# Kernel optimization log

Hardware: AMD Instinct MI355X
Metric: run time of the kernel (lower is better)

## Reference

```python
import jax, jax.numpy as jnp
import numpy as np

N = 100000
E = 1600000
F_IN = 4
HID = 8
HEADS = 8
NEG_SLOPE = 0.2


def setup_inputs() -> dict:
    key = jax.random.key(0)
    ks = jax.random.split(key, 12)
    x = jax.random.normal(ks[0], (N, F_IN), dtype=jnp.float32)
    edge_index = jax.random.randint(ks[1], (2, E), 0, N, dtype=jnp.int64)
    s = 0.3
    W1 = jax.random.normal(ks[2], (F_IN, HEADS * HID), dtype=jnp.float32) * s
    att_src1 = jax.random.normal(ks[3], (HEADS, HID), dtype=jnp.float32) * s
    att_dst1 = jax.random.normal(ks[4], (HEADS, HID), dtype=jnp.float32) * s
    b1 = jnp.zeros((HEADS * HID,), dtype=jnp.float32)
    W2 = jax.random.normal(ks[5], (HEADS * HID, 1), dtype=jnp.float32) * s
    att_src2 = jax.random.normal(ks[6], (1, 1), dtype=jnp.float32) * s
    att_dst2 = jax.random.normal(ks[7], (1, 1), dtype=jnp.float32) * s
    b2 = jnp.zeros((1,), dtype=jnp.float32)
    return {"x": x, "edge_index": edge_index, "W1": W1, "att_src1": att_src1,
            "att_dst1": att_dst1, "b1": b1, "W2": W2, "att_src2": att_src2,
            "att_dst2": att_dst2, "b2": b2}


def gat_conv(x, src, dst, W, att_s, att_d, b, heads, out_ch, concat):
    n = x.shape[0]
    h = (x @ W).reshape(n, heads, out_ch)              # [N,H,C]
    a_s = jnp.sum(h * att_s, axis=-1)                  # [N,H]
    a_d = jnp.sum(h * att_d, axis=-1)                  # [N,H]
    e = jax.nn.leaky_relu(a_s[src] + a_d[dst], NEG_SLOPE)  # [E,H]
    # segment softmax over edges grouped by destination node
    m = jax.ops.segment_max(e, dst, num_segments=n)
    e = jnp.exp(e - m[dst])
    denom = jax.ops.segment_sum(e, dst, num_segments=n)
    alpha = e / (denom[dst] + 1e-16)                   # [E,H]
    msg = h[src] * alpha[..., None]                    # [E,H,C]
    out = jax.ops.segment_sum(msg, dst, num_segments=n)  # [N,H,C]
    out = out.reshape(n, heads * out_ch) if concat else out.mean(axis=1)
    return out + b


def reference(x, edge_index, W1, att_src1, att_dst1, b1, W2, att_src2, att_dst2, b2):
    n = x.shape[0]
    loops = jnp.arange(n, dtype=edge_index.dtype)
    src = jnp.concatenate([edge_index[0], loops])
    dst = jnp.concatenate([edge_index[1], loops])
    h = gat_conv(x, src, dst, W1, att_src1, att_dst1, b1, HEADS, HID, True)
    h = jax.nn.elu(h)
    out = gat_conv(h, src, dst, W2, att_src2, att_dst2, b2, 1, 1, False)
    return jax.nn.sigmoid(out)
```

## Files before the change

### kernel.cpp

```cpp
#include <hip/hip_runtime.h>

#define NN 100000
#define NE 1600000
#define NBKT 391
#define CAP 8192
#define TILE 4096
#define NTILE ((NE + TILE - 1) / TILE)
#define NEG 0.2f

__global__ __launch_bounds__(512) void kP1_tile(
    const int* __restrict__ ei, int* __restrict__ bcnt, unsigned* __restrict__ bpack)
{
    __shared__ unsigned sarr[TILE];
    __shared__ int lh[512], lsc[512], lgb[512];
    int t = threadIdx.x;
    int e0 = blockIdx.x * TILE;
    int n = NE - e0; if (n > TILE) n = TILE;

    lh[t] = 0;
    __syncthreads();
    for (int i = t; i < n; i += 512) {
        int d = ei[NE + e0 + i];
        atomicAdd(&lh[d >> 8], 1);
    }
    __syncthreads();
    lsc[t] = lh[t];
    __syncthreads();
    #pragma unroll
    for (int o = 1; o < 512; o <<= 1) {
        int u = (t >= o) ? lsc[t - o] : 0;
        __syncthreads();
        lsc[t] += u;
        __syncthreads();
    }
    if (t < NBKT && lh[t] > 0) lgb[t] = atomicAdd(&bcnt[t], lh[t]);
    __syncthreads();
    lh[t] = lsc[t] - lh[t];
    __syncthreads();
    for (int i = t; i < n; i += 512) {
        int s = ei[e0 + i], d = ei[NE + e0 + i];
        int b = d >> 8;
        int pos = atomicAdd(&lh[b], 1);
        sarr[pos] = ((unsigned)s << 8) | (unsigned)(d & 255);
    }
    __syncthreads();
    int wave = t >> 6, lane = t & 63;
    for (int b = wave; b < NBKT; b += 8) {
        int start = (b == 0) ? 0 : lsc[b - 1];
        int cntb = lsc[b] - start;
        if (cntb == 0) continue;
        int gb = lgb[b];
        unsigned* dstp = &bpack[(size_t)b * CAP];
        for (int j = lane; j < cntb; j += 64) {
            int gpos = gb + j;
            if (gpos < CAP) dstp[gpos] = sarr[start + j];
        }
    }
}

__global__ __launch_bounds__(512) void kP2_build(
    const int* __restrict__ bcnt, const unsigned* __restrict__ bpack,
    int2* __restrict__ rowsd, int* __restrict__ esrc)
{
    __shared__ int lh[256], lsc[256], lcur[256];
    int b = blockIdx.x;
    int t = threadIdx.x;
    int cnt = bcnt[b];
    if (cnt > CAP) cnt = CAP;
    const unsigned* bp = &bpack[(size_t)b * CAP];
    int base = b * CAP;
    if (t < 256) lh[t] = 0;
    __syncthreads();
    for (int i = t; i < cnt; i += 512)
        atomicAdd(&lh[bp[i] & 255u], 1);
    __syncthreads();
    if (t < 256) lsc[t] = lh[t];
    __syncthreads();
    #pragma unroll
    for (int o = 1; o < 256; o <<= 1) {
        int u = 0;
        if (t < 256 && t >= o) u = lsc[t - o];
        __syncthreads();
        if (t < 256) lsc[t] += u;
        __syncthreads();
    }
    if (t < 256) {
        int ex = lsc[t] - lh[t];
        lcur[t] = ex;
        int node = b * 256 + t;
        if (node < NN) rowsd[node] = make_int2(base + ex, lh[t]);
    }
    __syncthreads();
    for (int i = t; i < cnt; i += 512) {
        unsigned u = bp[i];
        int pos = atomicAdd(&lcur[u & 255u], 1);
        esrc[base + pos] = (int)(u >> 8);
    }
}

__global__ __launch_bounds__(256) void kE_l1agg(
    const int2* __restrict__ rowsd, const int* __restrict__ esrc,
    const float* __restrict__ x, const float* __restrict__ atts,
    const float* __restrict__ attd, const float* __restrict__ W1,
    const float* __restrict__ b1, const float* __restrict__ W2,
    float* __restrict__ h2)
{
    __shared__ float sus[32], sud[32];
    int t = threadIdx.x;
    if (t < 64) {
        int half = t >> 5;
        int i = t & 31;
        int hh = i >> 2, k = i & 3;
        const float* att = half ? attd : atts;
        float acc = 0.f;
        #pragma unroll
        for (int j = 0; j < 8; j++)
            acc += W1[k * 64 + hh * 8 + j] * att[hh * 8 + j];
        (half ? sud : sus)[hh * 4 + k] = acc;
    }
    __syncthreads();

    int grp = t >> 3;
    int h   = t & 7;
    int dst = blockIdx.x * 32 + grp;

    int2 rd = rowsd[dst];
    int start = rd.x, m = rd.y;

    float4 u  = *reinterpret_cast<const float4*>(&sus[h * 4]);
    float4 vd = *reinterpret_cast<const float4*>(&sud[h * 4]);
    float4 xd = *reinterpret_cast<const float4*>(&x[(size_t)dst * 4]);
    float adj = xd.x * vd.x + xd.y * vd.y + xd.z * vd.z + xd.w * vd.w;

    float a0 = fmaf(xd.x, u.x, fmaf(xd.y, u.y, fmaf(xd.z, u.z, fmaf(xd.w, u.w, adj))));
    a0 = fmaxf(a0, NEG * a0);
    float p0 = __expf(a0);
    float den = p0;
    float xa0 = p0 * xd.x, xa1 = p0 * xd.y, xa2 = p0 * xd.z, xa3 = p0 * xd.w;

    int j = 0;
    for (; j + 4 <= m; j += 4) {
        int s0 = esrc[start + j];
        int s1 = esrc[start + j + 1];
        int s2 = esrc[start + j + 2];
        int s3 = esrc[start + j + 3];
        float4 q0 = *reinterpret_cast<const float4*>(&x[(size_t)s0 * 4]);
        float4 q1 = *reinterpret_cast<const float4*>(&x[(size_t)s1 * 4]);
        float4 q2 = *reinterpret_cast<const float4*>(&x[(size_t)s2 * 4]);
        float4 q3 = *reinterpret_cast<const float4*>(&x[(size_t)s3 * 4]);
        float b0 = fmaf(q0.x, u.x, fmaf(q0.y, u.y, fmaf(q0.z, u.z, fmaf(q0.w, u.w, adj))));
        float b1v = fmaf(q1.x, u.x, fmaf(q1.y, u.y, fmaf(q1.z, u.z, fmaf(q1.w, u.w, adj))));
        float b2v = fmaf(q2.x, u.x, fmaf(q2.y, u.y, fmaf(q2.z, u.z, fmaf(q2.w, u.w, adj))));
        float b3v = fmaf(q3.x, u.x, fmaf(q3.y, u.y, fmaf(q3.z, u.z, fmaf(q3.w, u.w, adj))));
        b0  = fmaxf(b0,  NEG * b0);
        b1v = fmaxf(b1v, NEG * b1v);
        b2v = fmaxf(b2v, NEG * b2v);
        b3v = fmaxf(b3v, NEG * b3v);
        float pa = __expf(b0);
        float pb = __expf(b1v);
        float pc = __expf(b2v);
        float pd = __expf(b3v);
        den += (pa + pb) + (pc + pd);
        xa0 = fmaf(pa, q0.x, fmaf(pb, q1.x, fmaf(pc, q2.x, fmaf(pd, q3.x, xa0))));
        xa1 = fmaf(pa, q0.y, fmaf(pb, q1.y, fmaf(pc, q2.y, fmaf(pd, q3.y, xa1))));
        xa2 = fmaf(pa, q0.z, fmaf(pb, q1.z, fmaf(pc, q2.z, fmaf(pd, q3.z, xa2))));
        xa3 = fmaf(pa, q0.w, fmaf(pb, q1.w, fmaf(pc, q2.w, fmaf(pd, q3.w, xa3))));
    }
    for (; j < m; ++j) {
        int s0 = esrc[start + j];
        float4 q0 = *reinterpret_cast<const float4*>(&x[(size_t)s0 * 4]);
        float b0 = fmaf(q0.x, u.x, fmaf(q0.y, u.y, fmaf(q0.z, u.z, fmaf(q0.w, u.w, adj))));
        b0 = fmaxf(b0, NEG * b0);
        float pb = __expf(b0);
        den += pb;
        xa0 = fmaf(pb, q0.x, xa0);
        xa1 = fmaf(pb, q0.y, xa1);
        xa2 = fmaf(pb, q0.z, xa2);
        xa3 = fmaf(pb, q0.w, xa3);
    }

    int c0 = h * 8;
    float4 w0l = *reinterpret_cast<const float4*>(&W1[c0]);
    float4 w0h = *reinterpret_cast<const float4*>(&W1[c0 + 4]);
    float4 w1l = *reinterpret_cast<const float4*>(&W1[64 + c0]);
    float4 w1h = *reinterpret_cast<const float4*>(&W1[64 + c0 + 4]);
    float4 w2l = *reinterpret_cast<const float4*>(&W1[128 + c0]);
    float4 w2h = *reinterpret_cast<const float4*>(&W1[128 + c0 + 4]);
    float4 w3l = *reinterpret_cast<const float4*>(&W1[192 + c0]);
    float4 w3h = *reinterpret_cast<const float4*>(&W1[192 + c0 + 4]);
    float4 bbl = *reinterpret_cast<const float4*>(&b1[c0]);
    float4 bbh = *reinterpret_cast<const float4*>(&b1[c0 + 4]);
    float4 wwl = *reinterpret_cast<const float4*>(&W2[c0]);
    float4 wwh = *reinterpret_cast<const float4*>(&W2[c0 + 4]);
    float inv = 1.f / (den + 1e-16f);

    float acc = 0.f;
    {
        float v;
        v = (xa0*w0l.x + xa1*w1l.x + xa2*w2l.x + xa3*w3l.x)*inv + bbl.x;
        v = v > 0.f ? v : (__expf(v) - 1.f);  acc += v * wwl.x;
        v = (xa0*w0l.y + xa1*w1l.y + xa2*w2l.y + xa3*w3l.y)*inv + bbl.y;
        v = v > 0.f ? v : (__expf(v) - 1.f);  acc += v * wwl.y;
        v = (xa0*w0l.z + xa1*w1l.z + xa2*w2l.z + xa3*w3l.z)*inv + bbl.z;
        v = v > 0.f ? v : (__expf(v) - 1.f);  acc += v * wwl.z;
        v = (xa0*w0l.w + xa1*w1l.w + xa2*w2l.w + xa3*w3l.w)*inv + bbl.w;
        v = v > 0.f ? v : (__expf(v) - 1.f);  acc += v * wwl.w;
        v = (xa0*w0h.x + xa1*w1h.x + xa2*w2h.x + xa3*w3h.x)*inv + bbh.x;
        v = v > 0.f ? v : (__expf(v) - 1.f);  acc += v * wwh.x;
        v = (xa0*w0h.y + xa1*w1h.y + xa2*w2h.y + xa3*w3h.y)*inv + bbh.y;
        v = v > 0.f ? v : (__expf(v) - 1.f);  acc += v * wwh.y;
        v = (xa0*w0h.z + xa1*w1h.z + xa2*w2h.z + xa3*w3h.z)*inv + bbh.z;
        v = v > 0.f ? v : (__expf(v) - 1.f);  acc += v * wwh.z;
        v = (xa0*w0h.w + xa1*w1h.w + xa2*w2h.w + xa3*w3h.w)*inv + bbh.w;
        v = v > 0.f ? v : (__expf(v) - 1.f);  acc += v * wwh.w;
    }
    acc += __shfl_xor(acc, 1, 8);
    acc += __shfl_xor(acc, 2, 8);
    acc += __shfl_xor(acc, 4, 8);
    if (h == 0) h2[dst] = acc;
}

__global__ __launch_bounds__(256) void kF_l2agg(
    const int2* __restrict__ rowsd, const int* __restrict__ esrc,
    const float* __restrict__ h2, const float* __restrict__ as2,
    const float* __restrict__ ad2, const float* __restrict__ b2,
    float* __restrict__ out)
{
    int t = threadIdx.x;
    int grp = t >> 3;
    int sub = t & 7;
    int dst = blockIdx.x * 32 + grp;
    int2 rd = rowsd[dst];
    int start = rd.x, end = rd.x + rd.y;
    float a_s = as2[0], a_d = ad2[0];
    float hdv = h2[dst];
    float hd = hdv * a_d;

    float den = 0.f, num = 0.f;
    if (sub == 0) {
        float v = hdv * a_s + hd;
        v = fmaxf(v, NEG * v);
        float p = __expf(v);
        den = p;
        num = p * hdv;
    }
    int i = start + sub;
    for (; i + 24 < end; i += 32) {
        float hs0 = h2[esrc[i]];
        float hs1 = h2[esrc[i + 8]];
        float hs2 = h2[esrc[i + 16]];
        float hs3 = h2[esrc[i + 24]];
        float v0 = fmaf(hs0, a_s, hd);
        float v1 = fmaf(hs1, a_s, hd);
        float v2 = fmaf(hs2, a_s, hd);
        float v3 = fmaf(hs3, a_s, hd);
        v0 = fmaxf(v0, NEG * v0);
        v1 = fmaxf(v1, NEG * v1);
        v2 = fmaxf(v2, NEG * v2);
        v3 = fmaxf(v3, NEG * v3);
        float p0 = __expf(v0);
        float p1 = __expf(v1);
        float p2 = __expf(v2);
        float p3 = __expf(v3);
        den += (p0 + p1) + (p2 + p3);
        num = fmaf(p0, hs0, fmaf(p1, hs1, fmaf(p2, hs2, fmaf(p3, hs3, num))));
    }
    for (; i < end; i += 8) {
        float hs = h2[esrc[i]];
        float v = fmaf(hs, a_s, hd);
        v = fmaxf(v, NEG * v);
        float p = __expf(v);
        den += p;
        num = fmaf(p, hs, num);
    }
    den += __shfl_xor(den, 1, 8);
    num += __shfl_xor(num, 1, 8);
    den += __shfl_xor(den, 2, 8);
    num += __shfl_xor(num, 2, 8);
    den += __shfl_xor(den, 4, 8);
    num += __shfl_xor(num, 4, 8);
    if (sub == 0) {
        float v = num / (den + 1e-16f) + b2[0];
        out[dst] = 1.f / (1.f + __expf(-v));
    }
}

extern "C" void kernel_launch(void* const* d_in, const int* in_sizes, int n_in,
                              void* d_out, int out_size, void* d_ws, size_t ws_size,
                              hipStream_t stream) {
    const float* x     = (const float*)d_in[0];
    const int*   ei    = (const int*)d_in[1];
    const float* W1    = (const float*)d_in[2];
    const float* atts1 = (const float*)d_in[3];
    const float* attd1 = (const float*)d_in[4];
    const float* b1    = (const float*)d_in[5];
    const float* W2    = (const float*)d_in[6];
    const float* atts2 = (const float*)d_in[7];
    const float* attd2 = (const float*)d_in[8];
    const float* b2    = (const float*)d_in[9];
    float* out = (float*)d_out;

    float* w = (float*)d_ws;
    float* h2 = w;
    int*  ibase = (int*)(w + (size_t)NN);
    int2* rowsd = (int2*)ibase;
    int*  bcnt  = ibase + (size_t)2 * NN;
    int*  esrc  = ibase + (size_t)2 * NN + 512;
    unsigned* bpack = (unsigned*)(esrc + (size_t)NBKT * CAP);

    dim3 gG(NN / 32);

    hipMemsetAsync(bcnt, 0, NBKT * sizeof(int), stream);
    hipLaunchKernelGGL(kP1_tile, dim3(NTILE), dim3(512), 0, stream, ei, bcnt, bpack);
    hipLaunchKernelGGL(kP2_build, dim3(NBKT), dim3(512), 0, stream, bcnt, bpack, rowsd, esrc);
    hipLaunchKernelGGL(kE_l1agg, gG, dim3(256), 0, stream, rowsd, esrc, x, atts1, attd1, W1, b1, W2, h2);
    hipLaunchKernelGGL(kF_l2agg, gG, dim3(256), 0, stream, rowsd, esrc, h2, atts2, attd2, b2, out);
}
```

Baseline: 83.45 us.

## Compact CSR edge array, stage scatter in LDS, precompute attention projections once

Replaces the memset with a tiny prep kernel that zeroes bucket counts and computes the fused W1·att projection vectors once, so the aggregation kernel no longer recomputes them per block. The CSR build now derives each bucket's base offset with a prefix reduction over bucket counts. This makes the edge source array dense (NE entries) instead of padded per bucket. It also scatters into shared memory first and then writes to global coalesced, using 1024 threads per block. The cost is an extra per-block reduction and more LDS in the build kernel, and the rest of the pipeline reads a more compact, cache-friendlier edge list.

Result: faster. 76.17 us (-8.7%).

```diff
diff --git a/kernel.cpp b/kernel.cpp
--- a/kernel.cpp
+++ b/kernel.cpp
@@ -7,6 +7,26 @@
 #define TILE 4096
 #define NTILE ((NE + TILE - 1) / TILE)
 #define NEG 0.2f
+
+__global__ __launch_bounds__(512) void kU_prep(
+    const float* __restrict__ W1, const float* __restrict__ atts,
+    const float* __restrict__ attd, float* __restrict__ us, float* __restrict__ ud,
+    int* __restrict__ bcnt)
+{
+    int t = threadIdx.x;
+    if (t < NBKT) bcnt[t] = 0;
+    if (t < 64) {
+        int half = t >> 5;
+        int i = t & 31;
+        int h = i >> 2, k = i & 3;
+        const float* att = half ? attd : atts;
+        float acc = 0.f;
+        #pragma unroll
+        for (int j = 0; j < 8; j++)
+            acc += W1[k * 64 + h * 8 + j] * att[h * 8 + j];
+        (half ? ud : us)[h * 4 + k] = acc;
+    }
+}
 
 __global__ __launch_bounds__(512) void kP1_tile(
     const int* __restrict__ ei, int* __restrict__ bcnt, unsigned* __restrict__ bpack)
@@ -58,20 +78,29 @@
     }
 }
 
-__global__ __launch_bounds__(512) void kP2_build(
+__global__ __launch_bounds__(1024) void kP2_build(
     const int* __restrict__ bcnt, const unsigned* __restrict__ bpack,
     int2* __restrict__ rowsd, int* __restrict__ esrc)
 {
     __shared__ int lh[256], lsc[256], lcur[256];
+    __shared__ int sbs[512];
+    __shared__ int sarr[CAP];
     int b = blockIdx.x;
     int t = threadIdx.x;
+    if (t < 512) sbs[t] = (t < b) ? bcnt[t] : 0;
+    __syncthreads();
+    #pragma unroll
+    for (int o = 256; o > 0; o >>= 1) {
+        if (t < o) sbs[t] += sbs[t + o];
+        __syncthreads();
+    }
+    int base = sbs[0];
     int cnt = bcnt[b];
     if (cnt > CAP) cnt = CAP;
     const unsigned* bp = &bpack[(size_t)b * CAP];
-    int base = b * CAP;
     if (t < 256) lh[t] = 0;
     __syncthreads();
-    for (int i = t; i < cnt; i += 512)
+    for (int i = t; i < cnt; i += 1024)
         atomicAdd(&lh[bp[i] & 255u], 1);
     __syncthreads();
     if (t < 256) lsc[t] = lh[t];
@@ -91,35 +120,24 @@
         if (node < NN) rowsd[node] = make_int2(base + ex, lh[t]);
     }
     __syncthreads();
-    for (int i = t; i < cnt; i += 512) {
+    for (int i = t; i < cnt; i += 1024) {
         unsigned u = bp[i];
         int pos = atomicAdd(&lcur[u & 255u], 1);
-        esrc[base + pos] = (int)(u >> 8);
-    }
+        sarr[pos] = (int)(u >> 8);
+    }
+    __syncthreads();
+    for (int i = t; i < cnt; i += 1024)
+        esrc[base + i] = sarr[i];
 }
 
 __global__ __launch_bounds__(256) void kE_l1agg(
     const int2* __restrict__ rowsd, const int* __restrict__ esrc,
-    const float* __restrict__ x, const float* __restrict__ atts,
-    const float* __restrict__ attd, const float* __restrict__ W1,
+    const float* __restrict__ x, const float* __restrict__ us,
+    const float* __restrict__ ud, const float* __restrict__ W1,
     const float* __restrict__ b1, const float* __restrict__ W2,
     float* __restrict__ h2)
 {
-    __shared__ float sus[32], sud[32];
-    int t = threadIdx.x;
-    if (t < 64) {
-        int half = t >> 5;
-        int i = t & 31;
-        int hh = i >> 2, k = i & 3;
-        const float* att = half ? attd : atts;
-        float acc = 0.f;
-        #pragma unroll
-        for (int j = 0; j < 8; j++)
-            acc += W1[k * 64 + hh * 8 + j] * att[hh * 8 + j];
-        (half ? sud : sus)[hh * 4 + k] = acc;
-    }
-    __syncthreads();
-
+    int t = threadIdx.x;
     int grp = t >> 3;
     int h   = t & 7;
     int dst = blockIdx.x * 32 + grp;
@@ -127,8 +145,8 @@
     int2 rd = rowsd[dst];
     int start = rd.x, m = rd.y;
 
-    float4 u  = *reinterpret_cast<const float4*>(&sus[h * 4]);
-    float4 vd = *reinterpret_cast<const float4*>(&sud[h * 4]);
+    float4 u  = *reinterpret_cast<const float4*>(&us[h * 4]);
+    float4 vd = *reinterpret_cast<const float4*>(&ud[h * 4]);
     float4 xd = *reinterpret_cast<const float4*>(&x[(size_t)dst * 4]);
     float adj = xd.x * vd.x + xd.y * vd.y + xd.z * vd.z + xd.w * vd.w;
 
@@ -301,18 +319,20 @@
     float* out = (float*)d_out;
 
     float* w = (float*)d_ws;
-    float* h2 = w;
-    int*  ibase = (int*)(w + (size_t)NN);
+    float* us = w;
+    float* ud = w + 32;
+    float* h2 = w + 64;
+    int*  ibase = (int*)(w + 64 + (size_t)NN);
     int2* rowsd = (int2*)ibase;
     int*  bcnt  = ibase + (size_t)2 * NN;
     int*  esrc  = ibase + (size_t)2 * NN + 512;
-    unsigned* bpack = (unsigned*)(esrc + (size_t)NBKT * CAP);
+    unsigned* bpack = (unsigned*)(esrc + (size_t)NE);
 
     dim3 gG(NN / 32);
 
-    hipMemsetAsync(bcnt, 0, NBKT * sizeof(int), stream);
+    hipLaunchKernelGGL(kU_prep, dim3(1), dim3(512), 0, stream, W1, atts1, attd1, us, ud, bcnt);
     hipLaunchKernelGGL(kP1_tile, dim3(NTILE), dim3(512), 0, stream, ei, bcnt, bpack);
-    hipLaunchKernelGGL(kP2_build, dim3(NBKT), dim3(512), 0, stream, bcnt, bpack, rowsd, esrc);
-    hipLaunchKernelGGL(kE_l1agg, gG, dim3(256), 0, stream, rowsd, esrc, x, atts1, attd1, W1, b1, W2, h2);
+    hipLaunchKernelGGL(kP2_build, dim3(NBKT), dim3(1024), 0, stream, bcnt, bpack, rowsd, esrc);
+    hipLaunchKernelGGL(kE_l1agg, gG, dim3(256), 0, stream, rowsd, esrc, x, us, ud, W1, b1, W2, h2);
     hipLaunchKernelGGL(kF_l2agg, gG, dim3(256), 0, stream, rowsd, esrc, h2, atts2, attd2, b2, out);
 }
```
